# Optimization experiments

Measured on AMD Instinct MI355X. Metric: run time of the kernel, lower is better.

Reference implementation:

```python
import jax, jax.numpy as jnp
import numpy as np

N_NODES, N_EDGES = 50000, 800000
N_IN, E_IN, N_OUT, E_OUT = 64, 32, 64, 32


def _xavier(key, fan_in, fan_out):
    std = (2.0 / (fan_in + fan_out)) ** 0.5
    return jax.random.normal(key, (fan_in, fan_out), dtype=jnp.float32) * std


def setup_inputs() -> dict:
    key = jax.random.key(0)
    ks = jax.random.split(key, 10)
    return {
        "feat": jax.random.normal(ks[0], (N_NODES, N_IN), dtype=jnp.float32),
        "edge_feat": jax.random.normal(ks[1], (N_EDGES, E_IN), dtype=jnp.float32),
        "w_msg": _xavier(ks[2], N_IN + E_IN, N_OUT),
        "b_msg": jnp.zeros((N_OUT,), dtype=jnp.float32),
        "w_node": _xavier(ks[3], N_IN + N_OUT, N_OUT),
        "b_node": jnp.zeros((N_OUT,), dtype=jnp.float32),
        "w_edge": _xavier(ks[4], N_IN + N_OUT + E_IN, E_OUT),
        "b_edge": jnp.zeros((E_OUT,), dtype=jnp.float32),
        "src_idx": jax.random.randint(ks[5], (N_EDGES,), 0, N_NODES, dtype=jnp.int32),
        "dst_idx": jax.random.randint(ks[6], (N_EDGES,), 0, N_NODES, dtype=jnp.int32),
    }


def reference(feat, edge_feat, w_msg, b_msg, w_node, b_node, w_edge, b_edge, src_idx, dst_idx):
    n_nodes = feat.shape[0]
    # --- message: gather src + edge, linear, tanh --- [E, n_out]
    src_h = feat[src_idx]
    m = jnp.tanh(jnp.concatenate([src_h, edge_feat], axis=1) @ w_msg + b_msg)
    # --- scatter-mean into destination nodes --- [N, n_out]
    sums = jax.ops.segment_sum(m, dst_idx, num_segments=n_nodes)
    cnt = jax.ops.segment_sum(jnp.ones((m.shape[0], 1), m.dtype), dst_idx, num_segments=n_nodes)
    neigh = sums / jnp.maximum(cnt, 1.0)
    # --- node update: cat([neigh, h]) -> linear -> tanh (dropout = identity in eval) ---
    h = jnp.tanh(jnp.concatenate([neigh, feat], axis=1) @ w_node + b_node)
    # --- edge update: cat([src h, dst neigh(updated), edge h]) -> linear -> tanh ---
    e = jnp.tanh(jnp.concatenate([src_h, h[dst_idx], edge_feat], axis=1) @ w_edge + b_edge)
    return h, e
```

## Files before the change

kernel.cpp:

```cpp
#include <hip/hip_runtime.h>

#define NNODES 50000
#define NEDGES 800000
#define NPAD   50176
#define NTILE_E (NEDGES / 16)
#define NTILE_N (NNODES / 16)

typedef __attribute__((ext_vector_type(8))) short bf16x8;
typedef __attribute__((ext_vector_type(4))) float f32x4;

union ABu { bf16x8 v; uint4 u; };

__device__ __forceinline__ float fast_tanh(float x) {
    float e = __expf(2.0f * x);
    return 1.0f - 2.0f * __builtin_amdgcn_rcpf(e + 1.0f);
}

__device__ __forceinline__ unsigned pk_rne(float x, float y) {
    unsigned a = __float_as_uint(x), b = __float_as_uint(y);
    a = (a + 0x7fffu + ((a >> 16) & 1u)) >> 16;
    b = (b + 0x7fffu + ((b >> 16) & 1u)) >> 16;
    return a | (b << 16);
}
__device__ __forceinline__ unsigned pk_tr(float a, float b) {
    return __builtin_amdgcn_perm(__float_as_uint(b), __float_as_uint(a), 0x07060302);
}
__device__ __forceinline__ float bf16_lo(unsigned u) { return __uint_as_float(u << 16); }
__device__ __forceinline__ float bf16_hi(unsigned u) { return __uint_as_float(u & 0xffff0000u); }

__device__ __forceinline__ ABu make_afrag(const float* p) {
    float4 a = ((const float4*)p)[0];
    float4 b = ((const float4*)p)[1];
    ABu r;
    r.u.x = pk_tr(a.x, a.y); r.u.y = pk_tr(a.z, a.w);
    r.u.z = pk_tr(b.x, b.y); r.u.w = pk_tr(b.z, b.w);
    return r;
}

template <int LDN>
__device__ __forceinline__ ABu make_bfrag_u(const unsigned* wp) {
    ABu r;
    r.u.x = wp[0 * LDN]; r.u.y = wp[1 * LDN];
    r.u.z = wp[2 * LDN]; r.u.w = wp[3 * LDN];
    return r;
}

template <int KH, int N>
__device__ __forceinline__ void stage_w(const float* __restrict__ w, unsigned* wl_u) {
    for (int i = threadIdx.x; i < KH * N; i += 256) {
        const int kp = i / N, n = i % N;
        wl_u[i] = pk_rne(w[(2 * kp) * N + n], w[(2 * kp + 1) * N + n]);
    }
}

#define MFMA(a, b, c) __builtin_amdgcn_mfma_f32_16x16x32_bf16((a).v, (b).v, (c), 0, 0, 0)

__global__ __launch_bounds__(256) void hist_kernel(const int* __restrict__ dst_idx,
                                                   int* __restrict__ cnt,
                                                   int* __restrict__ rank) {
    const int base = (blockIdx.x * 256 + threadIdx.x) * 4;
    if (base + 4 <= NEDGES) {
        int4 d = *(const int4*)(dst_idx + base);
        int4 r;
        r.x = atomicAdd(&cnt[d.x], 1);
        r.y = atomicAdd(&cnt[d.y], 1);
        r.z = atomicAdd(&cnt[d.z], 1);
        r.w = atomicAdd(&cnt[d.w], 1);
        *(int4*)(rank + base) = r;
    } else {
        for (int i = base; i < NEDGES; ++i) rank[i] = atomicAdd(&cnt[dst_idx[i]], 1);
    }
}

__global__ __launch_bounds__(256) void scan1(const int* __restrict__ cnt,
                                             int* __restrict__ off,
                                             int* __restrict__ btot) {
    __shared__ int s[256];
    const int tid = threadIdx.x;
    const int g = blockIdx.x * 256 + tid;
    const int own = cnt[g];
    s[tid] = own;
    __syncthreads();
    for (int o = 1; o < 256; o <<= 1) {
        int v = (tid >= o) ? s[tid - o] : 0;
        __syncthreads();
        s[tid] += v;
        __syncthreads();
    }
    off[g] = s[tid] - own;
    if (tid == 255) btot[blockIdx.x] = s[255];
}

__global__ __launch_bounds__(256) void scan2(int* __restrict__ btot) {
    __shared__ int s[256];
    const int tid = threadIdx.x;
    const int own = btot[tid];
    s[tid] = own;
    __syncthreads();
    for (int o = 1; o < 256; o <<= 1) {
        int v = (tid >= o) ? s[tid - o] : 0;
        __syncthreads();
        s[tid] += v;
        __syncthreads();
    }
    btot[tid] = s[tid] - own;
}

__global__ __launch_bounds__(256) void scan3(int* __restrict__ off,
                                             const int* __restrict__ btot) {
    const int g = blockIdx.x * 256 + threadIdx.x;
    off[g] += btot[blockIdx.x];
}

__global__ __launch_bounds__(256) void rows_kernel(const int* __restrict__ dst_idx,
                                                   const int* __restrict__ off,
                                                   int* __restrict__ rank) {
    const int base = (blockIdx.x * 256 + threadIdx.x) * 4;
    if (base + 4 <= NEDGES) {
        int4 d = *(const int4*)(dst_idx + base);
        int4 r = *(const int4*)(rank + base);
        r.x += off[d.x];
        r.y += off[d.y];
        r.z += off[d.z];
        r.w += off[d.w];
        *(int4*)(rank + base) = r;
    } else {
        for (int i = base; i < NEDGES; ++i) rank[i] += off[dst_idx[i]];
    }
}

template <int KC, int NT>
__global__ __launch_bounds__(256) void proj_kernel(
    const float* __restrict__ in, const float* __restrict__ w,
    const float* __restrict__ bias, float* __restrict__ out) {
    constexpr int N = NT * 16;
    constexpr int K = KC * 32;
    __shared__ __align__(16) unsigned wl[(K / 2) * N];
    stage_w<K / 2, N>(w, wl);
    __syncthreads();

    const int lane = threadIdx.x & 63, wave = threadIdx.x >> 6;
    const int col = lane & 15, quad = lane >> 4;

    ABu bf[KC][NT];
#pragma unroll
    for (int kc = 0; kc < KC; ++kc)
#pragma unroll
        for (int nt = 0; nt < NT; ++nt)
            bf[kc][nt] = make_bfrag_u<N>(&wl[(kc * 16 + (quad << 2)) * N + nt * 16 + col]);

    float bi[NT];
#pragma unroll
    for (int nt = 0; nt < NT; ++nt) bi[nt] = bias ? bias[nt * 16 + col] : 0.f;

    const int nw = gridDim.x << 2;
    for (int t = (blockIdx.x << 2) + wave; t < NTILE_N; t += nw) {
        const int n0 = t << 4;
        const int n = n0 + col;
        ABu a[KC];
#pragma unroll
        for (int kc = 0; kc < KC; ++kc)
            a[kc] = make_afrag(in + (size_t)n * K + kc * 32 + (quad << 3));

        f32x4 acc[NT];
#pragma unroll
        for (int nt = 0; nt < NT; ++nt)
            acc[nt] = (f32x4){bi[nt], bi[nt], bi[nt], bi[nt]};
#pragma unroll
        for (int nt = 0; nt < NT; ++nt)
#pragma unroll
            for (int kc = 0; kc < KC; ++kc)
                acc[nt] = MFMA(a[kc], bf[kc][nt], acc[nt]);

#pragma unroll
        for (int i = 0; i < 4; ++i) {
            const int nr = n0 + (quad << 2) + i;
            if (NT == 4) {
                float4 o = {acc[0][i], acc[1][i], acc[2][i], acc[3][i]};
                *(float4*)(out + (size_t)nr * 64 + (col << 2)) = o;
            } else {
                float2 o = {acc[0][i], acc[1][i]};
                *(float2*)(out + (size_t)nr * 32 + (col << 1)) = o;
            }
        }
    }
}

struct MsgBuf { ABu a2; float4 f4[4]; int4 rows; };

__device__ __forceinline__ void msg_load(
    int t, int col, int quad,
    const float* __restrict__ edge_feat, const float* __restrict__ projm,
    const int* __restrict__ src_idx, const int* __restrict__ rows, MsgBuf& b) {
    const int e0 = t << 4;
    const int4 s4 = *(const int4*)(src_idx + e0 + (quad << 2));
    b.rows = *(const int4*)(rows + e0 + (quad << 2));
    b.a2 = make_afrag(edge_feat + (size_t)(e0 + col) * 32 + (quad << 3));
    b.f4[0] = *(const float4*)(projm + (size_t)s4.x * 64 + (col << 2));
    b.f4[1] = *(const float4*)(projm + (size_t)s4.y * 64 + (col << 2));
    b.f4[2] = *(const float4*)(projm + (size_t)s4.z * 64 + (col << 2));
    b.f4[3] = *(const float4*)(projm + (size_t)s4.w * 64 + (col << 2));
}

__device__ __forceinline__ void msg_comp(
    int col, const ABu (&bf)[4], const MsgBuf& b, unsigned* __restrict__ m_out) {
    f32x4 acc[4];
#pragma unroll
    for (int nt = 0; nt < 4; ++nt) acc[nt] = (f32x4){0.f, 0.f, 0.f, 0.f};
#pragma unroll
    for (int nt = 0; nt < 4; ++nt) acc[nt] = MFMA(b.a2, bf[nt], acc[nt]);
    const int rw[4] = {b.rows.x, b.rows.y, b.rows.z, b.rows.w};
#pragma unroll
    for (int i = 0; i < 4; ++i) {
        uint2 o;
        o.x = pk_rne(fast_tanh(acc[0][i] + b.f4[i].x), fast_tanh(acc[1][i] + b.f4[i].y));
        o.y = pk_rne(fast_tanh(acc[2][i] + b.f4[i].z), fast_tanh(acc[3][i] + b.f4[i].w));
        *(uint2*)(m_out + (size_t)rw[i] * 32 + (col << 1)) = o;
    }
}

__global__ __launch_bounds__(256) void msg_kernel(
    const float* __restrict__ edge_feat, const float* __restrict__ w_bot,
    const int* __restrict__ src_idx, const int* __restrict__ rows,
    const float* __restrict__ projm, unsigned* __restrict__ m_out) {
    __shared__ __align__(16) unsigned wl[16 * 64];
    stage_w<16, 64>(w_bot, wl);
    __syncthreads();

    const int lane = threadIdx.x & 63, wave = threadIdx.x >> 6;
    const int col = lane & 15, quad = lane >> 4;

    ABu bf[4];
#pragma unroll
    for (int nt = 0; nt < 4; ++nt)
        bf[nt] = make_bfrag_u<64>(&wl[(quad << 2) * 64 + nt * 16 + col]);

    const int nw = gridDim.x << 2;
    int t = (blockIdx.x << 2) + wave;
    if (t >= NTILE_E) return;
    MsgBuf A, B;
    msg_load(t, col, quad, edge_feat, projm, src_idx, rows, A);
    for (;;) {
        const int t2 = t + nw;
        if (t2 < NTILE_E)
            msg_load(t2, col, quad, edge_feat, projm, src_idx, rows, B);
        msg_comp(col, bf, A, m_out);
        if (t2 >= NTILE_E) return;
        const int t3 = t2 + nw;
        if (t3 < NTILE_E)
            msg_load(t3, col, quad, edge_feat, projm, src_idx, rows, A);
        msg_comp(col, bf, B, m_out);
        if (t3 >= NTILE_E) return;
        t = t3;
    }
}

__global__ __launch_bounds__(256) void gather_kernel(
    const unsigned* __restrict__ m,
    const int* __restrict__ off , const int* __restrict__ cnt,
    float* __restrict__ neigh) {
    const int wave = threadIdx.x >> 6;
    const int lane = threadIdx.x & 63;
    const int n = blockIdx.x * 4 + wave;
    if (n >= NNODES) return;
    const int c = cnt[n];
    const int o = off[n];
    const int q = lane & 7;
    const int g = lane >> 3;

    float s[8];
#pragma unroll
    for (int j = 0; j < 8; ++j) s[j] = 0.f;
    for (int r = g; r < c; r += 8) {
        const uint4 u = *(const uint4*)(m + (size_t)(o + r) * 32 + (q << 2));
        s[0] += bf16_lo(u.x); s[1] += bf16_hi(u.x);
        s[2] += bf16_lo(u.y); s[3] += bf16_hi(u.y);
        s[4] += bf16_lo(u.z); s[5] += bf16_hi(u.z);
        s[6] += bf16_lo(u.w); s[7] += bf16_hi(u.w);
    }
#pragma unroll
    for (int j = 0; j < 8; ++j) {
        s[j] += __shfl_xor(s[j], 8);
        s[j] += __shfl_xor(s[j], 16);
        s[j] += __shfl_xor(s[j], 32);
    }
    if (g == 0) {
        const float inv = __builtin_amdgcn_rcpf((float)max(c, 1));
        float4 o0 = {s[0] * inv, s[1] * inv, s[2] * inv, s[3] * inv};
        float4 o1 = {s[4] * inv, s[5] * inv, s[6] * inv, s[7] * inv};
        float* dst = neigh + (size_t)n * 64 + (q << 3);
        ((float4*)dst)[0] = o0;
        ((float4*)dst)[1] = o1;
    }
}

__device__ __forceinline__ int mapk(int ks) {
    return ks < 64 ? ((ks >> 2) + ((ks >> 1) & 1) * 32 + (ks & 1) * 16) : ks;
}

__global__ __launch_bounds__(256) void node_update(
    const float* __restrict__ feat,
    const float* __restrict__ w_node, const float* __restrict__ b_node,
    float* __restrict__ h) {
    __shared__ __align__(16) unsigned wl[64 * 64];
    for (int i = threadIdx.x; i < 64 * 64; i += 256) {
        const int kp = i >> 6, n = i & 63;
        wl[i] = pk_rne(w_node[mapk(2 * kp) * 64 + n], w_node[mapk(2 * kp + 1) * 64 + n]);
    }
    __syncthreads();

    const int lane = threadIdx.x & 63, wave = threadIdx.x >> 6;
    const int col = lane & 15, quad = lane >> 4;

    ABu bf[4][4];
#pragma unroll
    for (int kc = 0; kc < 4; ++kc)
#pragma unroll
        for (int nt = 0; nt < 4; ++nt)
            bf[kc][nt] = make_bfrag_u<64>(&wl[(kc * 16 + (quad << 2)) * 64 + nt * 16 + col]);

    float bias[4];
#pragma unroll
    for (int nt = 0; nt < 4; ++nt) bias[nt] = b_node[nt * 16 + col];

    const int nw = gridDim.x << 2;
    for (int t = (blockIdx.x << 2) + wave; t < NTILE_N; t += nw) {
        const int n0 = t << 4;
        const int n = n0 + col;
        ABu a0 = make_afrag(h + (size_t)n * 64 + quad * 8);
        ABu a1 = make_afrag(h + (size_t)n * 64 + 32 + quad * 8);
        ABu a2 = make_afrag(feat + (size_t)n * 64 + quad * 8);
        ABu a3 = make_afrag(feat + (size_t)n * 64 + 32 + quad * 8);

        f32x4 acc[4];
#pragma unroll
        for (int nt = 0; nt < 4; ++nt)
            acc[nt] = (f32x4){bias[nt], bias[nt], bias[nt], bias[nt]};
#pragma unroll
        for (int nt = 0; nt < 4; ++nt) {
            acc[nt] = MFMA(a0, bf[0][nt], acc[nt]);
            acc[nt] = MFMA(a1, bf[1][nt], acc[nt]);
            acc[nt] = MFMA(a2, bf[2][nt], acc[nt]);
            acc[nt] = MFMA(a3, bf[3][nt], acc[nt]);
        }
#pragma unroll
        for (int i = 0; i < 4; ++i) {
            const int nr = n0 + quad * 4 + i;
#pragma unroll
            for (int nt = 0; nt < 4; ++nt)
                h[(size_t)nr * 64 + nt * 16 + col] = fast_tanh(acc[nt][i]);
        }
    }
}

struct EBuf { ABu a4; float2 g1[4]; float2 g2[4]; };

__device__ __forceinline__ void edge_load(
    int t, int col, int quad,
    const float* __restrict__ edge_feat,
    const float* __restrict__ p1, const float* __restrict__ p2,
    const int* __restrict__ src_idx, const int* __restrict__ dst_idx, EBuf& b) {
    const int e0 = t << 4;
    const int4 s4 = *(const int4*)(src_idx + e0 + (quad << 2));
    const int4 d4 = *(const int4*)(dst_idx + e0 + (quad << 2));
    b.a4 = make_afrag(edge_feat + (size_t)(e0 + col) * 32 + (quad << 3));
    b.g1[0] = *(const float2*)(p1 + (size_t)s4.x * 32 + (col << 1));
    b.g1[1] = *(const float2*)(p1 + (size_t)s4.y * 32 + (col << 1));
    b.g1[2] = *(const float2*)(p1 + (size_t)s4.z * 32 + (col << 1));
    b.g1[3] = *(const float2*)(p1 + (size_t)s4.w * 32 + (col << 1));
    b.g2[0] = *(const float2*)(p2 + (size_t)d4.x * 32 + (col << 1));
    b.g2[1] = *(const float2*)(p2 + (size_t)d4.y * 32 + (col << 1));
    b.g2[2] = *(const float2*)(p2 + (size_t)d4.z * 32 + (col << 1));
    b.g2[3] = *(const float2*)(p2 + (size_t)d4.w * 32 + (col << 1));
}

__device__ __forceinline__ void edge_comp(
    int t, int col, int quad, const ABu (&bf)[2],
    const EBuf& b, float* __restrict__ e_out) {
    f32x4 acc[2];
#pragma unroll
    for (int nt = 0; nt < 2; ++nt) acc[nt] = (f32x4){0.f, 0.f, 0.f, 0.f};
#pragma unroll
    for (int nt = 0; nt < 2; ++nt) acc[nt] = MFMA(b.a4, bf[nt], acc[nt]);
    const int e0 = t << 4;
#pragma unroll
    for (int i = 0; i < 4; ++i) {
        const int er = e0 + (quad << 2) + i;
        e_out[(size_t)er * 32 + col] = fast_tanh(acc[0][i] + b.g1[i].x + b.g2[i].x);
        e_out[(size_t)er * 32 + 16 + col] = fast_tanh(acc[1][i] + b.g1[i].y + b.g2[i].y);
    }
}

__global__ __launch_bounds__(256) void edge_update(
    const float* __restrict__ edge_feat, const float* __restrict__ w3,
    const float* __restrict__ p1, const float* __restrict__ p2,
    const int* __restrict__ src_idx, const int* __restrict__ dst_idx,
    float* __restrict__ e_out) {
    __shared__ __align__(16) unsigned wl[16 * 32];
    stage_w<16, 32>(w3, wl);
    __syncthreads();

    const int lane = threadIdx.x & 63, wave = threadIdx.x >> 6;
    const int col = lane & 15, quad = lane >> 4;

    ABu bf[2];
#pragma unroll
    for (int nt = 0; nt < 2; ++nt)
        bf[nt] = make_bfrag_u<32>(&wl[(quad << 2) * 32 + nt * 16 + col]);

    const int nw = gridDim.x << 2;
    int t = (blockIdx.x << 2) + wave;
    if (t >= NTILE_E) return;
    EBuf A, B;
    edge_load(t, col, quad, edge_feat, p1, p2, src_idx, dst_idx, A);
    for (;;) {
        const int t2 = t + nw;
        if (t2 < NTILE_E)
            edge_load(t2, col, quad, edge_feat, p1, p2, src_idx, dst_idx, B);
        edge_comp(t, col, quad, bf, A, e_out);
        if (t2 >= NTILE_E) return;
        const int t3 = t2 + nw;
        if (t3 < NTILE_E)
            edge_load(t3, col, quad, edge_feat, p1, p2, src_idx, dst_idx, A);
        edge_comp(t2, col, quad, bf, B, e_out);
        if (t3 >= NTILE_E) return;
        t = t3;
    }
}

extern "C" void kernel_launch(void* const* d_in, const int* in_sizes, int n_in,
                              void* d_out, int out_size, void* d_ws, size_t ws_size,
                              hipStream_t stream) {
    const float* feat      = (const float*)d_in[0];
    const float* edge_feat = (const float*)d_in[1];
    const float* w_msg     = (const float*)d_in[2];
    const float* b_msg     = (const float*)d_in[3];
    const float* w_node    = (const float*)d_in[4];
    const float* b_node    = (const float*)d_in[5];
    const float* w_edge    = (const float*)d_in[6];
    const float* b_edge    = (const float*)d_in[7];
    const int*   src_idx   = (const int*)d_in[8];
    const int*   dst_idx   = (const int*)d_in[9];

    float* h = (float*)d_out;
    float* e = (float*)d_out + (size_t)NNODES * 64;
    unsigned* m = (unsigned*)e;
    float* projm = h;

    int* cnt  = (int*)d_ws;
    int* off  = cnt + NPAD;
    int* btot = off + NPAD;
    int* rank = btot + 256;
    float* p1 = (float*)(rank + NEDGES);
    float* p2 = p1 + (size_t)NNODES * 32;

    hipMemsetAsync(cnt, 0, NPAD * sizeof(int), stream);
    hipMemsetAsync(btot, 0, 256 * sizeof(int), stream);

    hist_kernel<<<(NEDGES / 4 + 255) / 256, 256, 0, stream>>>(dst_idx, cnt, rank);
    scan1<<<NPAD / 256, 256, 0, stream>>>(cnt, off, btot);
    scan2<<<1, 256, 0, stream>>>(btot);
    scan3<<<NPAD / 256, 256, 0, stream>>>(off, btot);
    rows_kernel<<<(NEDGES / 4 + 255) / 256, 256, 0, stream>>>(dst_idx, off, rank);
    proj_kernel<2, 4><<<256, 256, 0, stream>>>(feat, w_msg, b_msg, projm);
    msg_kernel<<<2500, 256, 0, stream>>>(edge_feat, w_msg + 64 * 64,
                                         src_idx, rank, projm, m);
    gather_kernel<<<NNODES / 4, 256, 0, stream>>>(m, off, cnt, h);
    node_update<<<512, 256, 0, stream>>>(feat, w_node, b_node, h);
    proj_kernel<2, 2><<<256, 256, 0, stream>>>(feat, w_edge, b_edge, p1);
    proj_kernel<2, 2><<<256, 256, 0, stream>>>(h, w_edge + 64 * 32, nullptr, p2);
    edge_update<<<2500, 256, 0, stream>>>(edge_feat, w_edge + 128 * 32,
                                          p1, p2, src_idx, dst_idx, e);
}
```

Before: 392.5 us.

## Fuse edge-feature projection into message kernel and merge node projections

Computes the edge_feat @ w_edge-bottom partial product inside the message kernel, which already loads edge_feat fragments, and stores it as bf16 to a workspace buffer. The final edge pass then only gathers p1/p2 and adds them, with no reload of edge_feat and no MFMA. The two feat projections (message and edge) are merged into one kernel that reads feat once. This adds a 51MB bf16 intermediate write and read, plus bf16 rounding of the partial sum. The new path only runs when the workspace is large enough.

```diff
diff --git a/kernel.cpp b/kernel.cpp
--- a/kernel.cpp
+++ b/kernel.cpp
@@ -129,6 +129,72 @@
     }
 }
 
+__global__ __launch_bounds__(256) void proj2_kernel(
+    const float* __restrict__ feat,
+    const float* __restrict__ w_m, const float* __restrict__ b_m,
+    const float* __restrict__ w_e, const float* __restrict__ b_e,
+    float* __restrict__ projm, float* __restrict__ p1) {
+    __shared__ __align__(16) unsigned wlm[32 * 64];
+    __shared__ __align__(16) unsigned wle[32 * 32];
+    stage_w<32, 64>(w_m, wlm);
+    stage_w<32, 32>(w_e, wle);
+    __syncthreads();
+
+    const int lane = threadIdx.x & 63, wave = threadIdx.x >> 6;
+    const int col = lane & 15, quad = lane >> 4;
+
+    ABu bfm[2][4], bfe[2][2];
+#pragma unroll
+    for (int kc = 0; kc < 2; ++kc) {
+#pragma unroll
+        for (int nt = 0; nt < 4; ++nt)
+            bfm[kc][nt] = make_bfrag_u<64>(&wlm[(kc * 16 + (quad << 2)) * 64 + nt * 16 + col]);
+#pragma unroll
+        for (int nt = 0; nt < 2; ++nt)
+            bfe[kc][nt] = make_bfrag_u<32>(&wle[(kc * 16 + (quad << 2)) * 32 + nt * 16 + col]);
+    }
+
+    float bim[4], bie[2];
+#pragma unroll
+    for (int nt = 0; nt < 4; ++nt) bim[nt] = b_m[nt * 16 + col];
+#pragma unroll
+    for (int nt = 0; nt < 2; ++nt) bie[nt] = b_e[nt * 16 + col];
+
+    const int nw = gridDim.x << 2;
+    for (int t = (blockIdx.x << 2) + wave; t < NTILE_N; t += nw) {
+        const int n0 = t << 4;
+        const int n = n0 + col;
+        ABu a0 = make_afrag(feat + (size_t)n * 64 + (quad << 3));
+        ABu a1 = make_afrag(feat + (size_t)n * 64 + 32 + (quad << 3));
+
+        f32x4 accm[4], acce[2];
+#pragma unroll
+        for (int nt = 0; nt < 4; ++nt)
+            accm[nt] = (f32x4){bim[nt], bim[nt], bim[nt], bim[nt]};
+#pragma unroll
+        for (int nt = 0; nt < 2; ++nt)
+            acce[nt] = (f32x4){bie[nt], bie[nt], bie[nt], bie[nt]};
+#pragma unroll
+        for (int nt = 0; nt < 4; ++nt) {
+            accm[nt] = MFMA(a0, bfm[0][nt], accm[nt]);
+            accm[nt] = MFMA(a1, bfm[1][nt], accm[nt]);
+        }
+#pragma unroll
+        for (int nt = 0; nt < 2; ++nt) {
+            acce[nt] = MFMA(a0, bfe[0][nt], acce[nt]);
+            acce[nt] = MFMA(a1, bfe[1][nt], acce[nt]);
+        }
+#pragma unroll
+        for (int i = 0; i < 4; ++i) {
+            const int nr = n0 + (quad << 2) + i;
+            float4 om = {accm[0][i], accm[1][i], accm[2][i], accm[3][i]};
+            *(float4*)(projm + (size_t)nr * 64 + (col << 2)) = om;
+            float2 oe = {acce[0][i], acce[1][i]};
+            *(float2*)(p1 + (size_t)nr * 32 + (col << 1)) = oe;
+        }
+    }
+}
+
 template <int KC, int NT>
 __global__ __launch_bounds__(256) void proj_kernel(
     const float* __restrict__ in, const float* __restrict__ w,
@@ -202,8 +268,10 @@
     b.f4[3] = *(const float4*)(projm + (size_t)s4.w * 64 + (col << 2));
 }
 
+template <bool WQ3>
 __device__ __forceinline__ void msg_comp(
-    int col, const ABu (&bf)[4], const MsgBuf& b, unsigned* __restrict__ m_out) {
+    int t, int col, int quad, const ABu (&bf)[4], const ABu (&bf3)[2],
+    const MsgBuf& b, unsigned* __restrict__ m_out, unsigned* __restrict__ q3_out) {
     f32x4 acc[4];
 #pragma unroll
     for (int nt = 0; nt < 4; ++nt) acc[nt] = (f32x4){0.f, 0.f, 0.f, 0.f};
@@ -217,23 +285,44 @@
         o.y = pk_rne(fast_tanh(acc[2][i] + b.f4[i].z), fast_tanh(acc[3][i] + b.f4[i].w));
         *(uint2*)(m_out + (size_t)rw[i] * 32 + (col << 1)) = o;
     }
-}
-
+    if (WQ3) {
+        f32x4 a3[2];
+#pragma unroll
+        for (int nt = 0; nt < 2; ++nt) a3[nt] = (f32x4){0.f, 0.f, 0.f, 0.f};
+#pragma unroll
+        for (int nt = 0; nt < 2; ++nt) a3[nt] = MFMA(b.a2, bf3[nt], a3[nt]);
+        const int e0 = t << 4;
+#pragma unroll
+        for (int i = 0; i < 4; ++i)
+            q3_out[(size_t)(e0 + (quad << 2) + i) * 16 + col] = pk_rne(a3[0][i], a3[1][i]);
+    }
+}
+
+template <bool WQ3>
 __global__ __launch_bounds__(256) void msg_kernel(
     const float* __restrict__ edge_feat, const float* __restrict__ w_bot,
+    const float* __restrict__ w3,
     const int* __restrict__ src_idx, const int* __restrict__ rows,
-    const float* __restrict__ projm, unsigned* __restrict__ m_out) {
+    const float* __restrict__ projm, unsigned* __restrict__ m_out,
+    unsigned* __restrict__ q3_out) {
     __shared__ __align__(16) unsigned wl[16 * 64];
+    __shared__ __align__(16) unsigned wl3[16 * 32];
     stage_w<16, 64>(w_bot, wl);
+    if (WQ3) stage_w<16, 32>(w3, wl3);
     __syncthreads();
 
     const int lane = threadIdx.x & 63, wave = threadIdx.x >> 6;
     const int col = lane & 15, quad = lane >> 4;
 
-    ABu bf[4];
+    ABu bf[4], bf3[2];
 #pragma unroll
     for (int nt = 0; nt < 4; ++nt)
         bf[nt] = make_bfrag_u<64>(&wl[(quad << 2) * 64 + nt * 16 + col]);
+    if (WQ3) {
+#pragma unroll
+        for (int nt = 0; nt < 2; ++nt)
+            bf3[nt] = make_bfrag_u<32>(&wl3[(quad << 2) * 32 + nt * 16 + col]);
+    }
 
     const int nw = gridDim.x << 2;
     int t = (blockIdx.x << 2) + wave;
@@ -244,12 +333,12 @@
         const int t2 = t + nw;
         if (t2 < NTILE_E)
             msg_load(t2, col, quad, edge_feat, projm, src_idx, rows, B);
-        msg_comp(col, bf, A, m_out);
+        msg_comp<WQ3>(t, col, quad, bf, bf3, A, m_out, q3_out);
         if (t2 >= NTILE_E) return;
         const int t3 = t2 + nw;
         if (t3 < NTILE_E)
             msg_load(t3, col, quad, edge_feat, projm, src_idx, rows, A);
-        msg_comp(col, bf, B, m_out);
+        msg_comp<WQ3>(t2, col, quad, bf, bf3, B, m_out, q3_out);
         if (t3 >= NTILE_E) return;
         t = t3;
     }
@@ -350,6 +439,23 @@
             for (int nt = 0; nt < 4; ++nt)
                 h[(size_t)nr * 64 + nt * 16 + col] = fast_tanh(acc[nt][i]);
         }
+    }
+}
+
+__global__ __launch_bounds__(256) void edge_final(
+    const unsigned* __restrict__ q3, const float* __restrict__ p1,
+    const float* __restrict__ p2, const int* __restrict__ src_idx,
+    const int* __restrict__ dst_idx, float* __restrict__ e_out) {
+    const int stride = gridDim.x * 256;
+    for (int tid = blockIdx.x * 256 + threadIdx.x; tid < NEDGES * 16; tid += stride) {
+        const int e = tid >> 4, col = tid & 15;
+        const int src = src_idx[e];
+        const int dst = dst_idx[e];
+        const unsigned q = q3[tid];
+        const float2 g1 = *(const float2*)(p1 + (size_t)src * 32 + (col << 1));
+        const float2 g2 = *(const float2*)(p2 + (size_t)dst * 32 + (col << 1));
+        e_out[(size_t)e * 32 + col]      = fast_tanh(bf16_lo(q) + g1.x + g2.x);
+        e_out[(size_t)e * 32 + 16 + col] = fast_tanh(bf16_hi(q) + g1.y + g2.y);
     }
 }
 
@@ -453,6 +559,11 @@
     int* rank = btot + 256;
     float* p1 = (float*)(rank + NEDGES);
     float* p2 = p1 + (size_t)NNODES * 32;
+    unsigned* q3 = (unsigned*)(p2 + (size_t)NNODES * 32);
+
+    const size_t ws_need = (size_t)NPAD * 8 + 1024 + (size_t)NEDGES * 4 +
+                           (size_t)NNODES * 32 * 8 + (size_t)NEDGES * 16 * 4;
+    const bool big_ws = ws_size >= ws_need;
 
     hipMemsetAsync(cnt, 0, NPAD * sizeof(int), stream);
     hipMemsetAsync(btot, 0, 256 * sizeof(int), stream);
@@ -462,13 +573,23 @@
     scan2<<<1, 256, 0, stream>>>(btot);
     scan3<<<NPAD / 256, 256, 0, stream>>>(off, btot);
     rows_kernel<<<(NEDGES / 4 + 255) / 256, 256, 0, stream>>>(dst_idx, off, rank);
-    proj_kernel<2, 4><<<256, 256, 0, stream>>>(feat, w_msg, b_msg, projm);
-    msg_kernel<<<2500, 256, 0, stream>>>(edge_feat, w_msg + 64 * 64,
-                                         src_idx, rank, projm, m);
+    proj2_kernel<<<256, 256, 0, stream>>>(feat, w_msg, b_msg, w_edge, b_edge, projm, p1);
+    if (big_ws) {
+        msg_kernel<true><<<2500, 256, 0, stream>>>(edge_feat, w_msg + 64 * 64,
+                                                   w_edge + 128 * 32, src_idx, rank,
+                                                   projm, m, q3);
+    } else {
+        msg_kernel<false><<<2500, 256, 0, stream>>>(edge_feat, w_msg + 64 * 64,
+                                                    nullptr, src_idx, rank,
+                                                    projm, m, nullptr);
+    }
     gather_kernel<<<NNODES / 4, 256, 0, stream>>>(m, off, cnt, h);
     node_update<<<512, 256, 0, stream>>>(feat, w_node, b_node, h);
-    proj_kernel<2, 2><<<256, 256, 0, stream>>>(feat, w_edge, b_edge, p1);
     proj_kernel<2, 2><<<256, 256, 0, stream>>>(h, w_edge + 64 * 32, nullptr, p2);
-    edge_update<<<2500, 256, 0, stream>>>(edge_feat, w_edge + 128 * 32,
-                                          p1, p2, src_idx, dst_idx, e);
-}
+    if (big_ws) {
+        edge_final<<<4096, 256, 0, stream>>>(q3, p1, p2, src_idx, dst_idx, e);
+    } else {
+        edge_update<<<2500, 256, 0, stream>>>(edge_feat, w_edge + 128 * 32,
+                                              p1, p2, src_idx, dst_idx, e);
+    }
+}
```

Result: no change. 399.2 us (+1.7%).

## Fuse scan stages, node projections, and gather with node update into fewer kernels

Applied to the files above, without the earlier changes.

Merges scan2 and scan3 into one kernel where every block redoes the small block-total scan. Merges the two feat projections into a single proj2 kernel that reads feat once. Fuses the neighbour gather, node update and h projection into one gnode kernel, so the mean goes straight into MFMA A-fragments and h is transposed through shared memory for the p2 projection. This removes several launches and the round trip of neigh and h through global memory, but gnode now gathers with one lane per node per quad. That serialises over the degree and may cause load imbalance and less memory-level parallelism than the old eight-row-per-wave gather. The tail-handling loops are also dropped, which is safe only because NEDGES is divisible by 4.

```diff
diff --git a/kernel.cpp b/kernel.cpp
--- a/kernel.cpp
+++ b/kernel.cpp
@@ -67,8 +67,6 @@
         r.z = atomicAdd(&cnt[d.z], 1);
         r.w = atomicAdd(&cnt[d.w], 1);
         *(int4*)(rank + base) = r;
-    } else {
-        for (int i = base; i < NEDGES; ++i) rank[i] = atomicAdd(&cnt[dst_idx[i]], 1);
     }
 }
 
@@ -91,11 +89,11 @@
     if (tid == 255) btot[blockIdx.x] = s[255];
 }
 
-__global__ __launch_bounds__(256) void scan2(int* __restrict__ btot) {
+__global__ __launch_bounds__(256) void scan3b(int* __restrict__ off,
+                                              const int* __restrict__ btot) {
     __shared__ int s[256];
     const int tid = threadIdx.x;
-    const int own = btot[tid];
-    s[tid] = own;
+    s[tid] = btot[tid];
     __syncthreads();
     for (int o = 1; o < 256; o <<= 1) {
         int v = (tid >= o) ? s[tid - o] : 0;
@@ -103,13 +101,8 @@
         s[tid] += v;
         __syncthreads();
     }
-    btot[tid] = s[tid] - own;
-}
-
-__global__ __launch_bounds__(256) void scan3(int* __restrict__ off,
-                                             const int* __restrict__ btot) {
-    const int g = blockIdx.x * 256 + threadIdx.x;
-    off[g] += btot[blockIdx.x];
+    const int add = (blockIdx.x == 0) ? 0 : s[blockIdx.x - 1];
+    off[blockIdx.x * 256 + tid] += add;
 }
 
 __global__ __launch_bounds__(256) void rows_kernel(const int* __restrict__ dst_idx,
@@ -124,64 +117,71 @@
         r.z += off[d.z];
         r.w += off[d.w];
         *(int4*)(rank + base) = r;
-    } else {
-        for (int i = base; i < NEDGES; ++i) rank[i] += off[dst_idx[i]];
-    }
-}
-
-template <int KC, int NT>
-__global__ __launch_bounds__(256) void proj_kernel(
-    const float* __restrict__ in, const float* __restrict__ w,
-    const float* __restrict__ bias, float* __restrict__ out) {
-    constexpr int N = NT * 16;
-    constexpr int K = KC * 32;
-    __shared__ __align__(16) unsigned wl[(K / 2) * N];
-    stage_w<K / 2, N>(w, wl);
+    }
+}
+
+__global__ __launch_bounds__(256) void proj2_kernel(
+    const float* __restrict__ feat,
+    const float* __restrict__ w_m, const float* __restrict__ b_m,
+    const float* __restrict__ w_e, const float* __restrict__ b_e,
+    float* __restrict__ projm, float* __restrict__ p1) {
+    __shared__ __align__(16) unsigned wlm[32 * 64];
+    __shared__ __align__(16) unsigned wle[32 * 32];
+    stage_w<32, 64>(w_m, wlm);
+    stage_w<32, 32>(w_e, wle);
     __syncthreads();
 
     const int lane = threadIdx.x & 63, wave = threadIdx.x >> 6;
     const int col = lane & 15, quad = lane >> 4;
 
-    ABu bf[KC][NT];
-#pragma unroll
-    for (int kc = 0; kc < KC; ++kc)
-#pragma unroll
-        for (int nt = 0; nt < NT; ++nt)
-            bf[kc][nt] = make_bfrag_u<N>(&wl[(kc * 16 + (quad << 2)) * N + nt * 16 + col]);
-
-    float bi[NT];
-#pragma unroll
-    for (int nt = 0; nt < NT; ++nt) bi[nt] = bias ? bias[nt * 16 + col] : 0.f;
+    ABu bfm[2][4], bfe[2][2];
+#pragma unroll
+    for (int kc = 0; kc < 2; ++kc) {
+#pragma unroll
+        for (int nt = 0; nt < 4; ++nt)
+            bfm[kc][nt] = make_bfrag_u<64>(&wlm[(kc * 16 + (quad << 2)) * 64 + nt * 16 + col]);
+#pragma unroll
+        for (int nt = 0; nt < 2; ++nt)
+            bfe[kc][nt] = make_bfrag_u<32>(&wle[(kc * 16 + (quad << 2)) * 32 + nt * 16 + col]);
+    }
+
+    float bim[4], bie[2];
+#pragma unroll
+    for (int nt = 0; nt < 4; ++nt) bim[nt] = b_m[nt * 16 + col];
+#pragma unroll
+    for (int nt = 0; nt < 2; ++nt) bie[nt] = b_e[nt * 16 + col];
 
     const int nw = gridDim.x << 2;
     for (int t = (blockIdx.x << 2) + wave; t < NTILE_N; t += nw) {
         const int n0 = t << 4;
         const int n = n0 + col;
-        ABu a[KC];
-#pragma unroll
-        for (int kc = 0; kc < KC; ++kc)
-            a[kc] = make_afrag(in + (size_t)n * K + kc * 32 + (quad << 3));
-
-        f32x4 acc[NT];
-#pragma unroll
-        for (int nt = 0; nt < NT; ++nt)
-            acc[nt] = (f32x4){bi[nt], bi[nt], bi[nt], bi[nt]};
-#pragma unroll
-        for (int nt = 0; nt < NT; ++nt)
-#pragma unroll
-            for (int kc = 0; kc < KC; ++kc)
-                acc[nt] = MFMA(a[kc], bf[kc][nt], acc[nt]);
-
+        ABu a0 = make_afrag(feat + (size_t)n * 64 + (quad << 3));
+        ABu a1 = make_afrag(feat + (size_t)n * 64 + 32 + (quad << 3));
+
+        f32x4 accm[4], acce[2];
+#pragma unroll
+        for (int nt = 0; nt < 4; ++nt)
+            accm[nt] = (f32x4){bim[nt], bim[nt], bim[nt], bim[nt]};
+#pragma unroll
+        for (int nt = 0; nt < 2; ++nt)
+            acce[nt] = (f32x4){bie[nt], bie[nt], bie[nt], bie[nt]};
+#pragma unroll
+        for (int nt = 0; nt < 4; ++nt) {
+            accm[nt] = MFMA(a0, bfm[0][nt], accm[nt]);
+            accm[nt] = MFMA(a1, bfm[1][nt], accm[nt]);
+        }
+#pragma unroll
+        for (int nt = 0; nt < 2; ++nt) {
+            acce[nt] = MFMA(a0, bfe[0][nt], acce[nt]);
+            acce[nt] = MFMA(a1, bfe[1][nt], acce[nt]);
+        }
 #pragma unroll
         for (int i = 0; i < 4; ++i) {
             const int nr = n0 + (quad << 2) + i;
-            if (NT == 4) {
-                float4 o = {acc[0][i], acc[1][i], acc[2][i], acc[3][i]};
-                *(float4*)(out + (size_t)nr * 64 + (col << 2)) = o;
-            } else {
-                float2 o = {acc[0][i], acc[1][i]};
-                *(float2*)(out + (size_t)nr * 32 + (col << 1)) = o;
-            }
+            float4 om = {accm[0][i], accm[1][i], accm[2][i], accm[3][i]};
+            *(float4*)(projm + (size_t)nr * 64 + (col << 2)) = om;
+            float2 oe = {acce[0][i], acce[1][i]};
+            *(float2*)(p1 + (size_t)nr * 32 + (col << 1)) = oe;
         }
     }
 }
@@ -255,101 +255,114 @@
     }
 }
 
-__global__ __launch_bounds__(256) void gather_kernel(
-    const unsigned* __restrict__ m,
-    const int* __restrict__ off , const int* __restrict__ cnt,
-    float* __restrict__ neigh) {
-    const int wave = threadIdx.x >> 6;
-    const int lane = threadIdx.x & 63;
-    const int n = blockIdx.x * 4 + wave;
-    if (n >= NNODES) return;
-    const int c = cnt[n];
-    const int o = off[n];
-    const int q = lane & 7;
-    const int g = lane >> 3;
-
-    float s[8];
-#pragma unroll
-    for (int j = 0; j < 8; ++j) s[j] = 0.f;
-    for (int r = g; r < c; r += 8) {
-        const uint4 u = *(const uint4*)(m + (size_t)(o + r) * 32 + (q << 2));
-        s[0] += bf16_lo(u.x); s[1] += bf16_hi(u.x);
-        s[2] += bf16_lo(u.y); s[3] += bf16_hi(u.y);
-        s[4] += bf16_lo(u.z); s[5] += bf16_hi(u.z);
-        s[6] += bf16_lo(u.w); s[7] += bf16_hi(u.w);
-    }
-#pragma unroll
-    for (int j = 0; j < 8; ++j) {
-        s[j] += __shfl_xor(s[j], 8);
-        s[j] += __shfl_xor(s[j], 16);
-        s[j] += __shfl_xor(s[j], 32);
-    }
-    if (g == 0) {
-        const float inv = __builtin_amdgcn_rcpf((float)max(c, 1));
-        float4 o0 = {s[0] * inv, s[1] * inv, s[2] * inv, s[3] * inv};
-        float4 o1 = {s[4] * inv, s[5] * inv, s[6] * inv, s[7] * inv};
-        float* dst = neigh + (size_t)n * 64 + (q << 3);
-        ((float4*)dst)[0] = o0;
-        ((float4*)dst)[1] = o1;
-    }
-}
-
 __device__ __forceinline__ int mapk(int ks) {
     return ks < 64 ? ((ks >> 2) + ((ks >> 1) & 1) * 32 + (ks & 1) * 16) : ks;
 }
 
-__global__ __launch_bounds__(256) void node_update(
-    const float* __restrict__ feat,
+__global__ __launch_bounds__(256) void gnode_kernel(
+    const float* __restrict__ feat, const unsigned* __restrict__ m,
+    const int* __restrict__ off, const int* __restrict__ cnt,
     const float* __restrict__ w_node, const float* __restrict__ b_node,
-    float* __restrict__ h) {
+    const float* __restrict__ w2,
+    float* __restrict__ h, float* __restrict__ p2) {
     __shared__ __align__(16) unsigned wl[64 * 64];
+    __shared__ __align__(16) unsigned wl2[32 * 32];
+    __shared__ float tr[4][16 * 68];
+
     for (int i = threadIdx.x; i < 64 * 64; i += 256) {
         const int kp = i >> 6, n = i & 63;
         wl[i] = pk_rne(w_node[mapk(2 * kp) * 64 + n], w_node[mapk(2 * kp + 1) * 64 + n]);
     }
+    stage_w<32, 32>(w2, wl2);
     __syncthreads();
 
     const int lane = threadIdx.x & 63, wave = threadIdx.x >> 6;
     const int col = lane & 15, quad = lane >> 4;
 
-    ABu bf[4][4];
-#pragma unroll
-    for (int kc = 0; kc < 4; ++kc)
-#pragma unroll
-        for (int nt = 0; nt < 4; ++nt)
-            bf[kc][nt] = make_bfrag_u<64>(&wl[(kc * 16 + (quad << 2)) * 64 + nt * 16 + col]);
-
-    float bias[4];
-#pragma unroll
-    for (int nt = 0; nt < 4; ++nt) bias[nt] = b_node[nt * 16 + col];
-
-    const int nw = gridDim.x << 2;
-    for (int t = (blockIdx.x << 2) + wave; t < NTILE_N; t += nw) {
-        const int n0 = t << 4;
-        const int n = n0 + col;
-        ABu a0 = make_afrag(h + (size_t)n * 64 + quad * 8);
-        ABu a1 = make_afrag(h + (size_t)n * 64 + 32 + quad * 8);
-        ABu a2 = make_afrag(feat + (size_t)n * 64 + quad * 8);
-        ABu a3 = make_afrag(feat + (size_t)n * 64 + 32 + quad * 8);
-
-        f32x4 acc[4];
-#pragma unroll
-        for (int nt = 0; nt < 4; ++nt)
-            acc[nt] = (f32x4){bias[nt], bias[nt], bias[nt], bias[nt]};
+    int t = blockIdx.x * 4 + wave;
+    if (t > NTILE_N - 1) t = NTILE_N - 1;
+    const int n0 = t << 4;
+    const int n = n0 + col;
+    const int c = cnt[n];
+    const int o = off[n];
+
+    float s0[8], s1[8];
+#pragma unroll
+    for (int j = 0; j < 8; ++j) { s0[j] = 0.f; s1[j] = 0.f; }
+    for (int r = 0; r < c; ++r) {
+        const unsigned* rp = m + (size_t)(o + r) * 32;
+        const uint4 u0 = *(const uint4*)(rp + (quad << 2));
+        const uint4 u1 = *(const uint4*)(rp + 16 + (quad << 2));
+        s0[0] += bf16_lo(u0.x); s0[1] += bf16_hi(u0.x);
+        s0[2] += bf16_lo(u0.y); s0[3] += bf16_hi(u0.y);
+        s0[4] += bf16_lo(u0.z); s0[5] += bf16_hi(u0.z);
+        s0[6] += bf16_lo(u0.w); s0[7] += bf16_hi(u0.w);
+        s1[0] += bf16_lo(u1.x); s1[1] += bf16_hi(u1.x);
+        s1[2] += bf16_lo(u1.y); s1[3] += bf16_hi(u1.y);
+        s1[4] += bf16_lo(u1.z); s1[5] += bf16_hi(u1.z);
+        s1[6] += bf16_lo(u1.w); s1[7] += bf16_hi(u1.w);
+    }
+    const float inv = __builtin_amdgcn_rcpf((float)max(c, 1));
+    ABu a0, a1;
+    a0.u.x = pk_tr(s0[0] * inv, s0[1] * inv); a0.u.y = pk_tr(s0[2] * inv, s0[3] * inv);
+    a0.u.z = pk_tr(s0[4] * inv, s0[5] * inv); a0.u.w = pk_tr(s0[6] * inv, s0[7] * inv);
+    a1.u.x = pk_tr(s1[0] * inv, s1[1] * inv); a1.u.y = pk_tr(s1[2] * inv, s1[3] * inv);
+    a1.u.z = pk_tr(s1[4] * inv, s1[5] * inv); a1.u.w = pk_tr(s1[6] * inv, s1[7] * inv);
+    const ABu a2 = make_afrag(feat + (size_t)n * 64 + (quad << 3));
+    const ABu a3 = make_afrag(feat + (size_t)n * 64 + 32 + (quad << 3));
+
+    f32x4 acc[4];
+#pragma unroll
+    for (int nt = 0; nt < 4; ++nt) {
+        const float bi = b_node[nt * 16 + col];
+        acc[nt] = (f32x4){bi, bi, bi, bi};
+    }
+#pragma unroll
+    for (int nt = 0; nt < 4; ++nt) {
+        acc[nt] = MFMA(a0, make_bfrag_u<64>(&wl[((quad << 2)) * 64 + nt * 16 + col]), acc[nt]);
+        acc[nt] = MFMA(a1, make_bfrag_u<64>(&wl[(16 + (quad << 2)) * 64 + nt * 16 + col]), acc[nt]);
+        acc[nt] = MFMA(a2, make_bfrag_u<64>(&wl[(32 + (quad << 2)) * 64 + nt * 16 + col]), acc[nt]);
+        acc[nt] = MFMA(a3, make_bfrag_u<64>(&wl[(48 + (quad << 2)) * 64 + nt * 16 + col]), acc[nt]);
+    }
+
+    float* trw = tr[wave];
+#pragma unroll
+    for (int i = 0; i < 4; ++i) {
+        const int nr = n0 + (quad << 2) + i;
 #pragma unroll
         for (int nt = 0; nt < 4; ++nt) {
-            acc[nt] = MFMA(a0, bf[0][nt], acc[nt]);
-            acc[nt] = MFMA(a1, bf[1][nt], acc[nt]);
-            acc[nt] = MFMA(a2, bf[2][nt], acc[nt]);
-            acc[nt] = MFMA(a3, bf[3][nt], acc[nt]);
+            const float ht = fast_tanh(acc[nt][i]);
+            h[(size_t)nr * 64 + nt * 16 + col] = ht;
+            trw[((quad << 2) + i) * 68 + nt * 16 + col] = ht;
         }
-#pragma unroll
-        for (int i = 0; i < 4; ++i) {
-            const int nr = n0 + quad * 4 + i;
-#pragma unroll
-            for (int nt = 0; nt < 4; ++nt)
-                h[(size_t)nr * 64 + nt * 16 + col] = fast_tanh(acc[nt][i]);
-        }
+    }
+    __syncthreads();
+
+    float f[8], g[8];
+#pragma unroll
+    for (int j = 0; j < 8; ++j) {
+        f[j] = trw[col * 68 + (quad << 3) + j];
+        g[j] = trw[col * 68 + 32 + (quad << 3) + j];
+    }
+    ABu aT0, aT1;
+    aT0.u.x = pk_tr(f[0], f[1]); aT0.u.y = pk_tr(f[2], f[3]);
+    aT0.u.z = pk_tr(f[4], f[5]); aT0.u.w = pk_tr(f[6], f[7]);
+    aT1.u.x = pk_tr(g[0], g[1]); aT1.u.y = pk_tr(g[2], g[3]);
+    aT1.u.z = pk_tr(g[4], g[5]); aT1.u.w = pk_tr(g[6], g[7]);
+
+    f32x4 acc2[2];
+#pragma unroll
+    for (int nt = 0; nt < 2; ++nt) acc2[nt] = (f32x4){0.f, 0.f, 0.f, 0.f};
+#pragma unroll
+    for (int nt = 0; nt < 2; ++nt) {
+        acc2[nt] = MFMA(aT0, make_bfrag_u<32>(&wl2[((quad << 2)) * 32 + nt * 16 + col]), acc2[nt]);
+        acc2[nt] = MFMA(aT1, make_bfrag_u<32>(&wl2[(16 + (quad << 2)) * 32 + nt * 16 + col]), acc2[nt]);
+    }
+#pragma unroll
+    for (int i = 0; i < 4; ++i) {
+        const int nr = n0 + (quad << 2) + i;
+        float2 o2 = {acc2[0][i], acc2[1][i]};
+        *(float2*)(p2 + (size_t)nr * 32 + (col << 1)) = o2;
     }
 }
 
@@ -459,16 +472,14 @@
 
     hist_kernel<<<(NEDGES / 4 + 255) / 256, 256, 0, stream>>>(dst_idx, cnt, rank);
     scan1<<<NPAD / 256, 256, 0, stream>>>(cnt, off, btot);
-    scan2<<<1, 256, 0, stream>>>(btot);
-    scan3<<<NPAD / 256, 256, 0, stream>>>(off, btot);
+    scan3b<<<NPAD / 256, 256, 0, stream>>>(off, btot);
     rows_kernel<<<(NEDGES / 4 + 255) / 256, 256, 0, stream>>>(dst_idx, off, rank);
-    proj_kernel<2, 4><<<256, 256, 0, stream>>>(feat, w_msg, b_msg, projm);
+    proj2_kernel<<<256, 256, 0, stream>>>(feat, w_msg, b_msg, w_edge, b_edge, projm, p1);
     msg_kernel<<<2500, 256, 0, stream>>>(edge_feat, w_msg + 64 * 64,
                                          src_idx, rank, projm, m);
-    gather_kernel<<<NNODES / 4, 256, 0, stream>>>(m, off, cnt, h);
-    node_update<<<512, 256, 0, stream>>>(feat, w_node, b_node, h);
-    proj_kernel<2, 2><<<256, 256, 0, stream>>>(feat, w_edge, b_edge, p1);
-    proj_kernel<2, 2><<<256, 256, 0, stream>>>(h, w_edge + 64 * 32, nullptr, p2);
+    gnode_kernel<<<(NTILE_N + 3) / 4, 256, 0, stream>>>(feat, m, off, cnt,
+                                                        w_node, b_node,
+                                                        w_edge + 64 * 32, h, p2);
     edge_update<<<2500, 256, 0, stream>>>(edge_feat, w_edge + 128 * 32,
                                           p1, p2, src_idx, dst_idx, e);
 }
```

New measurement: 379.4 us. 3.4% less time.
